# Performance work log

Hardware: AMD Instinct MI355X
Metric: run time of the kernel (lower is better)

## Reference

```python
import jax, jax.numpy as jnp
import numpy as np

B, S = 256, 500
NQ, DQ, DV, M, F = 10000, 128, 256, 50, 512


def _kaiming(key, shape, fan_in):
    return jax.random.normal(key, shape, dtype=jnp.float32) * np.sqrt(2.0 / fan_in)


def setup_inputs() -> dict:
    key = jax.random.key(0)
    ks = jax.random.split(key, 24)
    inp = {
        'q_data': jax.random.randint(ks[0], (B, S), 0, NQ, dtype=jnp.int32),
        'qa_data': jax.random.randint(ks[1], (B, S), 0, 2 * NQ, dtype=jnp.int32),
        'target': jax.random.randint(ks[2], (B, S), 0, 3, dtype=jnp.int32),
        'time_data': jax.random.randint(ks[3], (B, S), 0, 9902, dtype=jnp.int32),
        'attempt_data': jax.random.randint(ks[4], (B, S), 0, 4000, dtype=jnp.int32),
        'hint_data': jax.random.randint(ks[5], (B, S), 0, 60, dtype=jnp.int32),
        'hintTotal_data': jax.random.randint(ks[6], (B, S), 0, 60, dtype=jnp.int32),
    }
    # embedding tables (padding row 0 zeroed, as in torch padding_idx=0)
    inp['q_emb'] = _kaiming(ks[7], (NQ + 1, DQ), DQ).at[0].set(0.0)
    inp['qa_emb'] = _kaiming(ks[8], (2 * NQ + 1, DV), DV).at[0].set(0.0)
    inp['time_emb'] = _kaiming(ks[9], (9902, DQ), DQ).at[0].set(0.0)
    inp['attempt_emb'] = _kaiming(ks[10], (4000, DQ), DQ).at[0].set(0.0)
    inp['hint_total_emb'] = _kaiming(ks[11], (60, DQ), DQ).at[0].set(0.0)
    # memory init
    inp['Mk'] = _kaiming(ks[12], (M, DQ), DQ)
    inp['Mv0'] = _kaiming(ks[13], (M, DV), DV)
    # difficulty linears (shared weights applied twice)
    inp['diff_W'] = _kaiming(ks[14], (DQ, DQ), DQ)
    inp['diff_b'] = jnp.zeros((DQ,), jnp.float32)
    inp['diff2_W'] = _kaiming(ks[15], (DQ, DQ), DQ)
    inp['diff2_b'] = jnp.zeros((DQ,), jnp.float32)
    # DKVMN write head: erase/add linears (DV -> DV)
    inp['erase_W'] = _kaiming(ks[16], (DV, DV), DV)
    inp['erase_b'] = jnp.zeros((DV,), jnp.float32)
    inp['add_W'] = _kaiming(ks[17], (DV, DV), DV)
    inp['add_b'] = jnp.zeros((DV,), jnp.float32)
    # readout
    inp['read_W'] = _kaiming(ks[18], (F, DV + DQ), DV + DQ)
    inp['read_b'] = jnp.zeros((F,), jnp.float32)
    inp['pred_W'] = _kaiming(ks[19], (1, F), F)
    inp['pred_b'] = jnp.zeros((1,), jnp.float32)
    return inp


def reference(q_data, qa_data, target, time_data, attempt_data, hint_data, hintTotal_data,
              q_emb, qa_emb, time_emb, attempt_emb, hint_total_emb,
              Mk, Mv0, diff_W, diff_b, diff2_W, diff2_b,
              erase_W, erase_b, add_W, add_b, read_W, read_b, pred_W, pred_b):
    lin1 = lambda x: x @ diff_W.T + diff_b
    lin2 = lambda x: x @ diff2_W.T + diff2_b

    qe = q_emb[q_data]                        # [B,S,DQ]
    te = time_emb[time_data]
    ae = attempt_emb[attempt_data]
    he = hint_total_emb[hint_data]            # forward uses hint_total_embed for both
    hte = hint_total_emb[hintTotal_data]

    time_final = jax.nn.sigmoid(lin2(jnp.tanh(lin1(te + qe))))
    diff_final = jax.nn.sigmoid(lin2(jnp.tanh(lin1(hte + he + ae + qe))))
    q_proc = lin1(qe + diff_final * (he + hte + ae))  # [B,S,DQ]
    qa_e = qa_emb[qa_data]                            # [B,S,DV]

    Mv_init = jnp.broadcast_to(Mv0[None], (q_data.shape[0], M, DV))

    def step(Mv, inp):
        q, qa = inp                                   # [B,DQ], [B,DV]
        w = jax.nn.softmax(q @ Mk.T, axis=-1)         # [B,M]
        read = jnp.einsum('bm,bmd->bd', w, Mv)        # [B,DV]
        e = jax.nn.sigmoid(qa @ erase_W.T + erase_b)  # [B,DV]
        a = jnp.tanh(qa @ add_W.T + add_b)            # [B,DV]
        Mv = Mv * (1.0 - w[:, :, None] * e[:, None, :]) + w[:, :, None] * a[:, None, :]
        return Mv, read

    _, reads = jax.lax.scan(step, Mv_init,
                            (jnp.swapaxes(q_proc, 0, 1), jnp.swapaxes(qa_e, 0, 1)))
    reads = jnp.swapaxes(reads, 0, 1)                 # [B,S,DV]

    input_embed = q_proc + time_final * te            # [B,S,DQ]
    predict_input = jnp.concatenate([reads, input_embed], axis=-1)
    rc = jnp.tanh(predict_input @ read_W.T + read_b)  # [B,S,F]
    pred = (rc @ pred_W.T + pred_b).reshape(-1)       # [B*S]

    t1 = target.reshape(-1)
    mask = t1 >= 1
    y = jnp.where(mask, t1 - 1, 0).astype(jnp.float32)
    # BCE with logits: log(1+e^x) - x*y
    lelem = jnp.logaddexp(0.0, pred) - pred * y
    n = jnp.maximum(jnp.sum(mask.astype(jnp.float32)), 1.0)
    loss = jnp.sum(jnp.where(mask, lelem, 0.0)) / n
    maskf = mask.astype(jnp.float32)
    return loss, jax.nn.sigmoid(pred) * maskf, y * maskf
```

## Files before the change

kernel.cpp:

```cpp
#include <hip/hip_runtime.h>
#include <cstdint>
#include <cstddef>

#define NB 256
#define SQ 500
#define NROWS (NB * SQ)
#define DQ 128
#define DV 256
#define MM 50
#define FF 512
#define NQA 20096
#define WSTRIDE 52
#define WT 10

typedef _Float16 half8 __attribute__((ext_vector_type(8)));
typedef float floatx4 __attribute__((ext_vector_type(4)));
typedef float f2 __attribute__((ext_vector_type(2)));
typedef unsigned int u32;
typedef unsigned short u16;

__device__ __forceinline__ float4 ld4(const float* p) {
    return *reinterpret_cast<const float4*>(p);
}
__device__ __forceinline__ float sigf(float x) { return 1.f / (1.f + __expf(-x)); }
__device__ __forceinline__ float tanhfast(float x) { return 2.f / (1.f + __expf(-2.f * x)) - 1.f; }
__device__ __forceinline__ int gmap(int l, int s0, int CS) {
    int b = (unsigned)l / (unsigned)CS;
    return b * SQ + s0 + (l - b * CS);
}
__device__ __forceinline__ void st4h(u16* dst, float4 v) {
    _Float16 h0 = (_Float16)v.x, h1 = (_Float16)v.y, h2 = (_Float16)v.z, h3 = (_Float16)v.w;
    ushort4 u;
    u.x = *(u16*)&h0; u.y = *(u16*)&h1; u.z = *(u16*)&h2; u.w = *(u16*)&h3;
    *(ushort4*)dst = u;
}
__device__ __forceinline__ float h2f(u16 b) { _Float16 h; *(u16*)&h = b; return (float)h; }
__device__ __forceinline__ u16 f2h(float x) { _Float16 h = (_Float16)x; return *(u16*)&h; }

__global__ __launch_bounds__(256) void cvt16(
    const float* __restrict__ s, u16* __restrict__ d, int n4)
{
    int i = blockIdx.x * 256 + threadIdx.x;
    if (i < n4) st4h(d + 4 * (size_t)i, ld4(s + 4 * (size_t)i));
}

__global__ __launch_bounds__(256) void mkcvt(
    const float* __restrict__ Mk, u16* __restrict__ Mkh)
{
    int i = blockIdx.x * 256 + threadIdx.x;
    if (i >= 64 * 32) return;
    int row = i >> 5;
    float4 v = (row < MM) ? ld4(Mk + (size_t)row * DQ + (i & 31) * 4)
                          : float4{0.f, 0.f, 0.f, 0.f};
    st4h(Mkh + 4 * (size_t)i, v);
}

__global__ __launch_bounds__(256) void prep128(
    const int* __restrict__ q_data, const int* __restrict__ time_data,
    const int* __restrict__ attempt_data, const int* __restrict__ hint_data,
    const int* __restrict__ hintT_data,
    const float* __restrict__ q_emb, const float* __restrict__ time_emb,
    const float* __restrict__ attempt_emb, const float* __restrict__ ht_emb,
    u16* __restrict__ Xp, u16* __restrict__ S3p, u16* __restrict__ QEp,
    int s0, int CS, int Nc)
{
    int g = blockIdx.x * 256 + threadIdx.x;
    int l = g >> 5;
    int kq = (g & 31) << 2;
    if (l >= Nc) return;
    int n = gmap(l, s0, CS);
    float4 qe  = ld4(q_emb       + (size_t)q_data[n]       * DQ + kq);
    float4 te  = ld4(time_emb    + (size_t)time_data[n]    * DQ + kq);
    float4 ae  = ld4(attempt_emb + (size_t)attempt_data[n] * DQ + kq);
    float4 he  = ld4(ht_emb      + (size_t)hint_data[n]    * DQ + kq);
    float4 hte = ld4(ht_emb      + (size_t)hintT_data[n]   * DQ + kq);
    size_t off = (size_t)l * DQ + kq;
    float4 x1, s3, x2;
    x1.x = te.x + qe.x; x1.y = te.y + qe.y; x1.z = te.z + qe.z; x1.w = te.w + qe.w;
    s3.x = he.x + hte.x + ae.x; s3.y = he.y + hte.y + ae.y;
    s3.z = he.z + hte.z + ae.z; s3.w = he.w + hte.w + ae.w;
    x2.x = s3.x + qe.x; x2.y = s3.y + qe.y; x2.z = s3.z + qe.z; x2.w = s3.w + qe.w;
    st4h(Xp + off, x1);
    st4h(Xp + (size_t)Nc * DQ + off, x2);
    st4h(S3p + off, s3);
    st4h(QEp + off, qe);
}

template <int MODE>
__global__ __launch_bounds__(256, 3) void gemm16(
    const u16* __restrict__ A, const u16* __restrict__ W0,
    const u16* __restrict__ W1, const float* __restrict__ b0,
    const float* __restrict__ b1, u16* __restrict__ Yh,
    float* __restrict__ Yf,
    const u16* __restrict__ QEp, const u16* __restrict__ S3p,
    const int* __restrict__ idx, const float* __restrict__ gtab,
    u16* __restrict__ AUX, const float* __restrict__ predW,
    int K, int Nc, int s0, int CS)
{
    __shared__ u16 smem[2 * 128 * 40];
    u16* At = smem;
    u16* Bt = smem + 128 * 40;
    const int tid = threadIdx.x;
    const int row0 = blockIdx.x * 128;
    const int by = blockIdx.y;

    const u16* Wp;
    int col0;
    if constexpr (MODE == 4) { Wp = (by < 2) ? W0 : W1; col0 = (by & 1) * 128; }
    else { Wp = W0; col0 = by * 128; }
    const float* bias = (MODE == 4 && by >= 2) ? b1 : b0;

    floatx4 acc[4][4];
#pragma unroll
    for (int m = 0; m < 4; ++m)
#pragma unroll
        for (int n = 0; n < 4; ++n) acc[m][n] = (floatx4)0.f;

    const int lane = tid & 63, wv = tid >> 6;
    const int wr = (wv >> 1) * 64, wc = (wv & 1) * 64;
    const int q = lane >> 4, c0 = lane & 15;

    for (int kt = 0; kt < K; kt += 32) {
#pragma unroll
        for (int i = 0; i < 4; ++i) {
            int c = tid + i * 256;
            if (c < 512) {
                int r = c >> 2, seg = c & 3;
                const u16* src = A + (size_t)(row0 + r) * K + kt + seg * 8;
                *(uint4*)&At[r * 40 + seg * 8] = *(const uint4*)src;
            } else {
                int cb = c - 512;
                int r = cb >> 2, seg = cb & 3;
                const u16* src = Wp + (size_t)(col0 + r) * K + kt + seg * 8;
                *(uint4*)&Bt[r * 40 + seg * 8] = *(const uint4*)src;
            }
        }
        __syncthreads();
        half8 af[4], bf[4];
#pragma unroll
        for (int m = 0; m < 4; ++m) af[m] = *(half8*)&At[(wr + m * 16 + c0) * 40 + q * 8];
#pragma unroll
        for (int n = 0; n < 4; ++n) bf[n] = *(half8*)&Bt[(wc + n * 16 + c0) * 40 + q * 8];
#pragma unroll
        for (int m = 0; m < 4; ++m)
#pragma unroll
            for (int n = 0; n < 4; ++n)
                acc[m][n] = __builtin_amdgcn_mfma_f32_16x16x32_f16(af[m], bf[n], acc[m][n], 0, 0, 0);
        __syncthreads();
    }

    float bv[4];
#pragma unroll
    for (int n = 0; n < 4; ++n) bv[n] = bias[col0 + wc + n * 16 + c0];

    if constexpr (MODE == 5) {
        float pw[4];
#pragma unroll
        for (int n = 0; n < 4; ++n) pw[n] = predW[col0 + wc + n * 16 + c0];
        float* red = (float*)smem;
#pragma unroll
        for (int m = 0; m < 4; ++m)
#pragma unroll
            for (int r4 = 0; r4 < 4; ++r4) {
                int row = wr + m * 16 + q * 4 + r4;
                float pp = 0.f;
#pragma unroll
                for (int n = 0; n < 4; ++n)
                    pp = fmaf(tanhfast(acc[m][n][r4] + bv[n]), pw[n], pp);
                red[row * 33 + (wv & 1) * 16 + c0] = pp;
            }
        __syncthreads();
        if (tid < 128) {
            float s = 0.f;
#pragma unroll
            for (int j = 0; j < 32; ++j) s += red[tid * 33 + j];
            atomicAdd(&Yf[row0 + tid], s);
        }
    } else {
#pragma unroll
        for (int m = 0; m < 4; ++m)
#pragma unroll
            for (int r4 = 0; r4 < 4; ++r4) {
                int row = row0 + wr + m * 16 + q * 4 + r4;
#pragma unroll
                for (int n = 0; n < 4; ++n) {
                    int col = col0 + wc + n * 16 + c0;
                    float v = acc[m][n][r4] + bv[n];
                    if constexpr (MODE == 1) {
                        Yh[(size_t)row * 128 + col] = f2h(tanhfast(v));
                    } else if constexpr (MODE == 2) {
                        v = sigf(v);
                        if (row < Nc) {
                            Yh[(size_t)row * 128 + col] = f2h(v);
                        } else {
                            size_t o = (size_t)(row - Nc) * 128 + col;
                            float qe = h2f(QEp[o]), s3 = h2f(S3p[o]);
                            Yh[(size_t)row * 128 + col] = f2h(fmaf(v, s3, qe));
                        }
                    } else if constexpr (MODE == 3) {
                        size_t o = (size_t)row * 128 + col;
                        float tf = h2f(Yh[o]);
                        float te = gtab[(size_t)idx[gmap(row, s0, CS)] * 128 + col];
                        AUX[(size_t)row * 384 + 256 + col] = f2h(fmaf(tf, te, v));
                        Yh[o] = f2h(v);
                    } else {
                        bool isE = (by < 2);
                        v = isE ? sigf(v) : tanhfast(v);
                        AUX[((size_t)row * 256 + col) * 2 + (isE ? 0 : 1)] = f2h(v);
                    }
                }
            }
    }
}

__global__ __launch_bounds__(256) void wsoftmax_mfma(
    const u16* __restrict__ QP, const u16* __restrict__ Mkh,
    float* __restrict__ Wb)
{
    __shared__ float Sred[128 * 67];
    u16* At = (u16*)Sred;
    u16* Bt = At + 128 * 40;
    const int tid = threadIdx.x;
    const int row0 = blockIdx.x * 128;
    const int lane = tid & 63, wv = tid >> 6;
    const int wr = wv * 32;
    const int q = lane >> 4, c0 = lane & 15;

    floatx4 acc[2][4];
#pragma unroll
    for (int m = 0; m < 2; ++m)
#pragma unroll
        for (int n = 0; n < 4; ++n) acc[m][n] = (floatx4)0.f;

    for (int kt = 0; kt < DQ; kt += 32) {
#pragma unroll
        for (int i = 0; i < 3; ++i) {
            int c = tid + i * 256;
            if (c < 512) {
                int r = c >> 2, seg = c & 3;
                *(uint4*)&At[r * 40 + seg * 8] =
                    *(const uint4*)(QP + (size_t)(row0 + r) * DQ + kt + seg * 8);
            } else {
                int cb = c - 512;
                int r = cb >> 2, seg = cb & 3;
                *(uint4*)&Bt[r * 40 + seg * 8] =
                    *(const uint4*)(Mkh + (size_t)r * DQ + kt + seg * 8);
            }
        }
        __syncthreads();
        half8 af[2], bf[4];
#pragma unroll
        for (int m = 0; m < 2; ++m) af[m] = *(half8*)&At[(wr + m * 16 + c0) * 40 + q * 8];
#pragma unroll
        for (int n = 0; n < 4; ++n) bf[n] = *(half8*)&Bt[(n * 16 + c0) * 40 + q * 8];
#pragma unroll
        for (int m = 0; m < 2; ++m)
#pragma unroll
            for (int n = 0; n < 4; ++n)
                acc[m][n] = __builtin_amdgcn_mfma_f32_16x16x32_f16(af[m], bf[n], acc[m][n], 0, 0, 0);
        __syncthreads();
    }

#pragma unroll
    for (int m = 0; m < 2; ++m)
#pragma unroll
        for (int r4 = 0; r4 < 4; ++r4) {
            int row = wr + m * 16 + q * 4 + r4;
#pragma unroll
            for (int n = 0; n < 4; ++n)
                Sred[row * 67 + n * 16 + c0] = acc[m][n][r4];
        }
    __syncthreads();

    if (tid < 128) {
        float* s = &Sred[tid * 67];
        float mx = -3.0e38f;
#pragma unroll
        for (int m = 0; m < MM; ++m) mx = fmaxf(mx, s[m]);
        float sum = 0.f;
#pragma unroll
        for (int m = 0; m < MM; ++m) { float e = __expf(s[m] - mx); s[m] = e; sum += e; }
        float inv = 1.f / sum;
#pragma unroll
        for (int m = 0; m < MM; ++m) s[m] *= inv;
        s[50] = 0.f; s[51] = 0.f;
    }
    __syncthreads();

    for (int i = tid; i < 128 * 13; i += 256) {
        int row = i / 13, seg = i - row * 13;
        float4 v;
        v.x = Sred[row * 67 + seg * 4 + 0];
        v.y = Sred[row * 67 + seg * 4 + 1];
        v.z = Sred[row * 67 + seg * 4 + 2];
        v.w = Sred[row * 67 + seg * 4 + 3];
        *(float4*)(Wb + (size_t)(row0 + row) * WSTRIDE + seg * 4) = v;
    }
}

__global__ __launch_bounds__(256, 1) void scan_kernel(
    const float* __restrict__ Wb, const int* __restrict__ qa_data,
    const u32* __restrict__ EAtab,
    const float* __restrict__ Mv0, float* __restrict__ MvSt,
    u16* __restrict__ RDIE, int CS, int s0, int first)
{
    __shared__ float wt[2][WT * WSTRIDE];
    const int b = blockIdx.x;
    const int d = threadIdx.x;

    f2 mv[25];
    if (first) {
#pragma unroll
        for (int j = 0; j < 25; ++j) {
            mv[j].x = Mv0[(2 * j) * DV + d];
            mv[j].y = Mv0[(2 * j + 1) * DV + d];
        }
    } else {
#pragma unroll
        for (int j = 0; j < 25; ++j) {
            mv[j].x = MvSt[((size_t)b * MM + 2 * j) * DV + d];
            mv[j].y = MvSt[((size_t)b * MM + 2 * j + 1) * DV + d];
        }
    }

    const float* wbase = Wb + (size_t)b * CS * WSTRIDE;
    const int* qap = qa_data + (size_t)b * SQ + s0;
    u16* rp = RDIE + (size_t)b * CS * 384 + d;

    const int NT = CS / WT;
    const bool loader = (d < (WT * WSTRIDE / 4));

    if (loader) *(float4*)&wt[0][d * 4] = ld4(wbase + d * 4);
    u32 ea[WT];
    {
        int qi[WT];
#pragma unroll
        for (int i = 0; i < WT; ++i) qi[i] = qap[i];
#pragma unroll
        for (int i = 0; i < WT; ++i) ea[i] = EAtab[(size_t)qi[i] * DV + d];
    }
    __syncthreads();

    int cur = 0;
    for (int tile = 0; tile < NT; ++tile) {
        float4 wreg;
        u32 ean[WT];
        const bool havenext = (tile + 1 < NT);
        if (havenext) {
            if (loader) wreg = ld4(wbase + (size_t)(tile + 1) * WT * WSTRIDE + d * 4);
            int qn[WT];
#pragma unroll
            for (int i = 0; i < WT; ++i) qn[i] = qap[(tile + 1) * WT + i];
#pragma unroll
            for (int i = 0; i < WT; ++i) ean[i] = EAtab[(size_t)qn[i] * DV + d];
        }

        float4 wpp[2][13];
#pragma unroll
        for (int i = 0; i < 13; ++i)
            wpp[0][i] = *(const float4*)&wt[cur][i * 4];

#pragma unroll
        for (int s = 0; s < WT; ++s) {
            if (s + 1 < WT) {
#pragma unroll
                for (int i = 0; i < 13; ++i)
                    wpp[(s + 1) & 1][i] =
                        *(const float4*)&wt[cur][(s + 1) * WSTRIDE + i * 4];
            }
            const f2* w2 = (const f2*)wpp[s & 1];
            u32 eav = ea[s];
            float e = h2f((u16)(eav & 0xffff));
            float a = h2f((u16)(eav >> 16));
            f2 e2; e2.x = e; e2.y = e;
            f2 a2; a2.x = a; a2.y = a;
            f2 r0 = (f2)0.f, r1 = (f2)0.f, r2 = (f2)0.f, r3 = (f2)0.f;
#pragma unroll
            for (int j = 0; j < 24; j += 4) {
                f2 w_0 = w2[j + 0], w_1 = w2[j + 1], w_2 = w2[j + 2], w_3 = w2[j + 3];
                r0 += w_0 * mv[j + 0];
                r1 += w_1 * mv[j + 1];
                r2 += w_2 * mv[j + 2];
                r3 += w_3 * mv[j + 3];
                f2 t0 = a2 - e2 * mv[j + 0];
                f2 t1 = a2 - e2 * mv[j + 1];
                f2 t2 = a2 - e2 * mv[j + 2];
                f2 t3 = a2 - e2 * mv[j + 3];
                mv[j + 0] += w_0 * t0;
                mv[j + 1] += w_1 * t1;
                mv[j + 2] += w_2 * t2;
                mv[j + 3] += w_3 * t3;
            }
            {
                f2 w24 = w2[24];
                r0 += w24 * mv[24];
                f2 t = a2 - e2 * mv[24];
                mv[24] += w24 * t;
            }
            f2 rs = (r0 + r1) + (r2 + r3);
            rp[(size_t)(tile * WT + s) * 384] = f2h(rs.x + rs.y);
        }

        if (havenext) {
            if (loader) *(float4*)&wt[1 - cur][d * 4] = wreg;
#pragma unroll
            for (int i = 0; i < WT; ++i) ea[i] = ean[i];
            __syncthreads();
            cur ^= 1;
        }
    }

#pragma unroll
    for (int j = 0; j < 25; ++j) {
        MvSt[((size_t)b * MM + 2 * j) * DV + d]     = mv[j].x;
        MvSt[((size_t)b * MM + 2 * j + 1) * DV + d] = mv[j].y;
    }
}

__global__ __launch_bounds__(256) void loss_part(
    const float* __restrict__ P, const int* __restrict__ target,
    const float* __restrict__ pred_b, float* __restrict__ out,
    float* __restrict__ R2, int s0, int CS, int Nc)
{
    int l = blockIdx.x * 256 + threadIdx.x;
    float le = 0.f, mf = 0.f;
    if (l < Nc) {
        int n = gmap(l, s0, CS);
        float p = P[l] + pred_b[0];
        int t = target[n];
        float y = (t >= 1) ? (float)(t - 1) : 0.f;
        float sig = 1.f / (1.f + __expf(-p));
        if (t >= 1) {
            mf = 1.f;
            le = fmaxf(p, 0.f) + log1pf(__expf(-fabsf(p))) - p * y;
        }
        out[1 + n] = sig * mf;
        out[1 + NROWS + n] = y * mf;
    }
#pragma unroll
    for (int off = 32; off; off >>= 1) {
        le += __shfl_down(le, off);
        mf += __shfl_down(mf, off);
    }
    __shared__ float sl[4], sm[4];
    int wid = threadIdx.x >> 6;
    if ((threadIdx.x & 63) == 0) { sl[wid] = le; sm[wid] = mf; }
    __syncthreads();
    if (threadIdx.x == 0) {
        atomicAdd(R2, sl[0] + sl[1] + sl[2] + sl[3]);
        atomicAdd(R2 + 1, sm[0] + sm[1] + sm[2] + sm[3]);
    }
}

__global__ void loss_fin(const float* __restrict__ R2, float* __restrict__ out)
{
    out[0] = R2[0] / fmaxf(R2[1], 1.f);
}

extern "C" void kernel_launch(void* const* d_in, const int* in_sizes, int n_in,
                              void* d_out, int out_size, void* d_ws, size_t ws_size,
                              hipStream_t stream)
{
    const int* q_data       = (const int*)d_in[0];
    const int* qa_data      = (const int*)d_in[1];
    const int* target       = (const int*)d_in[2];
    const int* time_data    = (const int*)d_in[3];
    const int* attempt_data = (const int*)d_in[4];
    const int* hint_data    = (const int*)d_in[5];
    const int* hintT_data   = (const int*)d_in[6];
    const float* q_emb    = (const float*)d_in[7];
    const float* qa_emb   = (const float*)d_in[8];
    const float* time_emb = (const float*)d_in[9];
    const float* att_emb  = (const float*)d_in[10];
    const float* ht_emb   = (const float*)d_in[11];
    const float* Mk       = (const float*)d_in[12];
    const float* Mv0      = (const float*)d_in[13];
    const float* diff_W   = (const float*)d_in[14];
    const float* diff_b   = (const float*)d_in[15];
    const float* diff2_W  = (const float*)d_in[16];
    const float* diff2_b  = (const float*)d_in[17];
    const float* erase_W  = (const float*)d_in[18];
    const float* erase_b  = (const float*)d_in[19];
    const float* add_W    = (const float*)d_in[20];
    const float* add_b    = (const float*)d_in[21];
    const float* read_W   = (const float*)d_in[22];
    const float* read_b   = (const float*)d_in[23];
    const float* pred_W   = (const float*)d_in[24];
    const float* pred_b   = (const float*)d_in[25];
    float* out = (float*)d_out;
    (void)in_sizes; (void)n_in; (void)out_size;

    static const int cs_opts[] = {500, 250, 100, 50, 20, 10};
    const size_t FIXED = 44700000ull;
    int CS = 0;
    for (int i = 0; i < 6; ++i) {
        size_t need = (size_t)NB * cs_opts[i] * 2016ull + FIXED;
        if (need <= ws_size) { CS = cs_opts[i]; break; }
    }
    if (CS == 0) return;
    const int NCH = SQ / CS;
    const int Nc = NB * CS;

    float* MvSt  = (float*)d_ws;
    float* wbuf  = MvSt + (size_t)NB * MM * DV;
    float* bufP  = wbuf + (size_t)Nc * WSTRIDE;
    float* bufR2 = bufP + Nc;
    u16*  Xp     = (u16*)(bufR2 + 4);
    u16*  S3p    = Xp + (size_t)2 * Nc * 128;
    u16*  QEp    = S3p + (size_t)Nc * 128;
    u16*  RDIE   = QEp + (size_t)Nc * 128;
    u16*  dWh    = RDIE + (size_t)Nc * 384;
    u16*  d2Wh   = dWh + 16384;
    u16*  eWh    = d2Wh + 16384;
    u16*  aWh    = eWh + 65536;
    u16*  rWh    = aWh + 65536;
    u16*  qaEh   = rWh + 196608;
    u16*  Mkh    = qaEh + 5120256;
    u32*  EAtab  = (u32*)(Mkh + 8192);

    cvt16<<<16, 256, 0, stream>>>(diff_W,  dWh,  16384 / 4);
    cvt16<<<16, 256, 0, stream>>>(diff2_W, d2Wh, 16384 / 4);
    cvt16<<<64, 256, 0, stream>>>(erase_W, eWh,  65536 / 4);
    cvt16<<<64, 256, 0, stream>>>(add_W,   aWh,  65536 / 4);
    cvt16<<<192, 256, 0, stream>>>(read_W, rWh,  196608 / 4);
    cvt16<<<5001, 256, 0, stream>>>(qa_emb, qaEh, 5120256 / 4);
    mkcvt<<<8, 256, 0, stream>>>(Mk, Mkh);
    hipMemsetAsync(bufR2, 0, 4 * sizeof(float), stream);

    gemm16<4><<<dim3(NQA / 128, 4), 256, 0, stream>>>(
        qaEh, eWh, aWh, erase_b, add_b, nullptr, nullptr,
        nullptr, nullptr, nullptr, nullptr, (u16*)EAtab, nullptr, 256, 0, 0, 0);

    for (int c = 0; c < NCH; ++c) {
        const int s0 = c * CS;

        prep128<<<Nc / 8, 256, 0, stream>>>(
            q_data, time_data, attempt_data, hint_data, hintT_data,
            q_emb, time_emb, att_emb, ht_emb, Xp, S3p, QEp, s0, CS, Nc);

        gemm16<1><<<dim3(2 * Nc / 128, 1), 256, 0, stream>>>(
            Xp, dWh, nullptr, diff_b, nullptr, Xp, nullptr,
            nullptr, nullptr, nullptr, nullptr, nullptr, nullptr, 128, Nc, s0, CS);
        gemm16<2><<<dim3(2 * Nc / 128, 1), 256, 0, stream>>>(
            Xp, d2Wh, nullptr, diff2_b, nullptr, Xp, nullptr,
            QEp, S3p, nullptr, nullptr, nullptr, nullptr, 128, Nc, s0, CS);
        gemm16<3><<<dim3(Nc / 128, 1), 256, 0, stream>>>(
            Xp + (size_t)Nc * 128, dWh, nullptr, diff_b, nullptr, Xp, nullptr,
            nullptr, nullptr, time_data, time_emb, RDIE, nullptr, 128, Nc, s0, CS);
        wsoftmax_mfma<<<Nc / 128, 256, 0, stream>>>(Xp, Mkh, wbuf);
        scan_kernel<<<NB, DV, 0, stream>>>(
            wbuf, qa_data, EAtab, Mv0, MvSt, RDIE, CS, s0, c == 0 ? 1 : 0);

        hipMemsetAsync(bufP, 0, (size_t)Nc * sizeof(float), stream);
        gemm16<5><<<dim3(Nc / 128, 4), 256, 0, stream>>>(
            RDIE, rWh, nullptr, read_b, nullptr, nullptr, bufP,
            nullptr, nullptr, nullptr, nullptr, nullptr, pred_W, 384, Nc, s0, CS);

        loss_part<<<Nc / 256, 256, 0, stream>>>(bufP, target, pred_b, out, bufR2, s0, CS, Nc);
    }

    loss_fin<<<1, 1, 0, stream>>>(bufR2, out);
}
```

Baseline: 722.5 us.

## Use direct global-to-LDS loads with XOR-swizzled 64-wide K tiles in GEMM

The fp16 MFMA GEMM now stages A and W tiles with the global_load_lds builtin, writing global memory straight into LDS instead of going through registers. The K tile grows from 32 to 64, which halves the number of barrier pairs, and the padded row layout is replaced by an XOR swizzle to avoid LDS bank conflicts. Shared memory per block grows, so the occupancy hint drops from 3 to 2 blocks. The epilogue's reuse of smem as a reduction buffer may depend on the layout, and reduced occupancy could hurt latency hiding.

```diff
diff --git a/kernel.cpp b/kernel.cpp
--- a/kernel.cpp
+++ b/kernel.cpp
@@ -18,6 +18,13 @@
 typedef float f2 __attribute__((ext_vector_type(2)));
 typedef unsigned int u32;
 typedef unsigned short u16;
+
+typedef __attribute__((address_space(1))) void gvoid;
+typedef __attribute__((address_space(3))) void lvoid;
+
+__device__ __forceinline__ void gl16(const u16* g, u16* l) {
+    __builtin_amdgcn_global_load_lds((gvoid*)g, (lvoid*)l, 16, 0, 0);
+}
 
 __device__ __forceinline__ float4 ld4(const float* p) {
     return *reinterpret_cast<const float4*>(p);
@@ -87,7 +94,7 @@
 }
 
 template <int MODE>
-__global__ __launch_bounds__(256, 3) void gemm16(
+__global__ __launch_bounds__(256, 2) void gemm16(
     const u16* __restrict__ A, const u16* __restrict__ W0,
     const u16* __restrict__ W1, const float* __restrict__ b0,
     const float* __restrict__ b1, u16* __restrict__ Yh,
@@ -97,9 +104,9 @@
     u16* __restrict__ AUX, const float* __restrict__ predW,
     int K, int Nc, int s0, int CS)
 {
-    __shared__ u16 smem[2 * 128 * 40];
+    __shared__ u16 smem[2 * 128 * 64];
     u16* At = smem;
-    u16* Bt = smem + 128 * 40;
+    u16* Bt = smem + 128 * 64;
     const int tid = threadIdx.x;
     const int row0 = blockIdx.x * 128;
     const int by = blockIdx.y;
@@ -120,32 +127,41 @@
     const int wr = (wv >> 1) * 64, wc = (wv & 1) * 64;
     const int q = lane >> 4, c0 = lane & 15;
 
-    for (int kt = 0; kt < K; kt += 32) {
-#pragma unroll
-        for (int i = 0; i < 4; ++i) {
-            int c = tid + i * 256;
-            if (c < 512) {
-                int r = c >> 2, seg = c & 3;
-                const u16* src = A + (size_t)(row0 + r) * K + kt + seg * 8;
-                *(uint4*)&At[r * 40 + seg * 8] = *(const uint4*)src;
-            } else {
-                int cb = c - 512;
-                int r = cb >> 2, seg = cb & 3;
-                const u16* src = Wp + (size_t)(col0 + r) * K + kt + seg * 8;
-                *(uint4*)&Bt[r * 40 + seg * 8] = *(const uint4*)src;
-            }
+    for (int kt = 0; kt < K; kt += 64) {
+#pragma unroll
+        for (int j = 0; j < 4; ++j) {
+            int f = tid + j * 256;
+            int r = f >> 3;
+            int lg = (f & 7) ^ (r & 7);
+            gl16(A + (size_t)(row0 + r) * K + kt + lg * 8, &At[f * 8]);
+        }
+#pragma unroll
+        for (int j = 0; j < 4; ++j) {
+            int f = tid + j * 256;
+            int r = f >> 3;
+            int lg = (f & 7) ^ (r & 7);
+            gl16(Wp + (size_t)(col0 + r) * K + kt + lg * 8, &Bt[f * 8]);
         }
         __syncthreads();
-        half8 af[4], bf[4];
-#pragma unroll
-        for (int m = 0; m < 4; ++m) af[m] = *(half8*)&At[(wr + m * 16 + c0) * 40 + q * 8];
-#pragma unroll
-        for (int n = 0; n < 4; ++n) bf[n] = *(half8*)&Bt[(wc + n * 16 + c0) * 40 + q * 8];
-#pragma unroll
-        for (int m = 0; m < 4; ++m)
-#pragma unroll
-            for (int n = 0; n < 4; ++n)
-                acc[m][n] = __builtin_amdgcn_mfma_f32_16x16x32_f16(af[m], bf[n], acc[m][n], 0, 0, 0);
+#pragma unroll
+        for (int kk = 0; kk < 2; ++kk) {
+            half8 af[4], bf[4];
+#pragma unroll
+            for (int m = 0; m < 4; ++m) {
+                int row = wr + m * 16 + c0;
+                af[m] = *(half8*)&At[row * 64 + ((((kk << 2) | q)) ^ (row & 7)) * 8];
+            }
+#pragma unroll
+            for (int n = 0; n < 4; ++n) {
+                int row = wc + n * 16 + c0;
+                bf[n] = *(half8*)&Bt[row * 64 + ((((kk << 2) | q)) ^ (row & 7)) * 8];
+            }
+#pragma unroll
+            for (int m = 0; m < 4; ++m)
+#pragma unroll
+                for (int n = 0; n < 4; ++n)
+                    acc[m][n] = __builtin_amdgcn_mfma_f32_16x16x32_f16(af[m], bf[n], acc[m][n], 0, 0, 0);
+        }
         __syncthreads();
     }
 
```

Result: faster. 686.6 us (-5.0%).
